# Performance work log

Hardware: AMD Instinct MI355X
Metric: run time of the kernel (lower is better)

## Reference

```python
import jax, jax.numpy as jnp
import numpy as np

N_SUBS = 64
INPUT_DIMS = 256
MIDDLE_DIMS = 128
OUTPUT_DIMS = 256
N = 131072


def setup_inputs() -> dict:
    key = jax.random.key(0)
    k1, k2 = jax.random.split(key)
    x = jax.random.normal(k1, (N, INPUT_DIMS), dtype=jnp.float32)
    sub = jax.random.randint(k2, (N,), 0, N_SUBS, dtype=jnp.int64 if jax.config.jax_enable_x64 else jnp.int32)
    # learned scalar params, initialized as in the torch module
    Gamma = jnp.ones((1,), jnp.float32) / (MIDDLE_DIMS * INPUT_DIMS)
    Lambda = jnp.ones((1,), jnp.float32) / (OUTPUT_DIMS * (INPUT_DIMS + MIDDLE_DIMS))
    return {"x": x, "sub": sub, "Gamma": Gamma, "Lambda": Lambda}


def reference(x, sub, Gamma, Lambda):
    # per-subject mean via fused segment reduction (replaces python loop)
    sums = jax.ops.segment_sum(x, sub, num_segments=N_SUBS)                      # [S, D_in]
    counts = jax.ops.segment_sum(jnp.ones((x.shape[0],), x.dtype), sub,
                                 num_segments=N_SUBS)[:, None]                    # [S, 1]
    # torch fallback for empty group: mean over row 0 of x
    means = jnp.where(counts > 0, sums / jnp.maximum(counts, 1), x[0][None, :])   # [S, D_in]
    # F.linear with rank-1 all-Gamma weight == Gamma * row-sum broadcast to middle dims
    s = jax.nn.relu(Gamma[0] * jnp.sum(means, axis=1, keepdims=True))             # [S, 1]
    stats = jnp.broadcast_to(s, (N_SUBS, MIDDLE_DIMS))                            # [S, D_mid]
    batch_stats = stats[sub]                                                      # [N, D_mid] gather
    cat = jnp.concatenate([x, batch_stats], axis=1)                               # [N, D_in+D_mid]
    o = jax.nn.relu(Lambda[0] * jnp.sum(cat, axis=1, keepdims=True))              # [N, 1]
    return jnp.broadcast_to(o, (x.shape[0], OUTPUT_DIMS))                         # [N, D_out]
```

## Files before the change

### kernel.cpp

```cpp
#include <hip/hip_runtime.h>

#define N_ROWS    131072
#define D_IN      256
#define D_MID     128
#define N_SUBS    64
#define K1_BLOCKS 4096
#define ROWS_PER_WAVE (N_ROWS / (K1_BLOCKS * 4))


__global__ __launch_bounds__(256) void k1_rowsum(const float* __restrict__ x,
                                                 float* __restrict__ rowsum,
                                                 float* __restrict__ bins) {
    if (blockIdx.x == 0 && threadIdx.x < 2 * N_SUBS) bins[threadIdx.x] = 0.0f;
    const int lane   = threadIdx.x & 63;
    const int waveId = blockIdx.x * 4 + (threadIdx.x >> 6);
    const int row0   = waveId * ROWS_PER_WAVE;
    const float4* __restrict__ xp = (const float4*)x;
    #pragma unroll
    for (int r = 0; r < ROWS_PER_WAVE; r += 4) {
        float4 a = xp[(size_t)(row0 + r + 0) * 64 + lane];
        float4 b = xp[(size_t)(row0 + r + 1) * 64 + lane];
        float4 c = xp[(size_t)(row0 + r + 2) * 64 + lane];
        float4 d = xp[(size_t)(row0 + r + 3) * 64 + lane];
        float s0 = (a.x + a.y) + (a.z + a.w);
        float s1 = (b.x + b.y) + (b.z + b.w);
        float s2 = (c.x + c.y) + (c.z + c.w);
        float s3 = (d.x + d.y) + (d.z + d.w);
        #pragma unroll
        for (int m = 32; m >= 1; m >>= 1) {
            s0 += __shfl_xor(s0, m, 64);
            s1 += __shfl_xor(s1, m, 64);
            s2 += __shfl_xor(s2, m, 64);
            s3 += __shfl_xor(s3, m, 64);
        }
        if (lane == 0)
            *(float4*)(rowsum + row0 + r) = make_float4(s0, s1, s2, s3);
    }
}

__global__ __launch_bounds__(256) void k2_group(const float* __restrict__ rowsum,
                                                const int* __restrict__ sub,
                                                float* __restrict__ gsum,
                                                float* __restrict__ gcnt) {
    __shared__ float ls[N_SUBS];
    __shared__ float lc[N_SUBS];
    if (threadIdx.x < N_SUBS) { ls[threadIdx.x] = 0.0f; lc[threadIdx.x] = 0.0f; }
    __syncthreads();
    int stride = gridDim.x * blockDim.x;
    for (int i = blockIdx.x * blockDim.x + threadIdx.x; i < N_ROWS; i += stride) {
        int g = sub[i];
        atomicAdd(&ls[g], rowsum[i]);
        atomicAdd(&lc[g], 1.0f);
    }
    __syncthreads();
    if (threadIdx.x < N_SUBS) {
        atomicAdd(&gsum[threadIdx.x], ls[threadIdx.x]);
        atomicAdd(&gcnt[threadIdx.x], lc[threadIdx.x]);
    }
}

__global__ __launch_bounds__(256) void k3_out(const float* __restrict__ rowsum,
                                              const int* __restrict__ sub,
                                              const float* __restrict__ gsum,
                                              const float* __restrict__ gcnt,
                                              const float* __restrict__ Gamma,
                                              const float* __restrict__ Lambda,
                                              float* __restrict__ out) {
    const int lane   = threadIdx.x & 63;
    const int waveId = blockIdx.x * 4 + (threadIdx.x >> 6);
    const int row0   = waveId * ROWS_PER_WAVE;
    const float G = Gamma[0], L = Lambda[0];
    const float rs0 = rowsum[0];
    #pragma unroll
    for (int r = 0; r < ROWS_PER_WAVE; ++r) {
        const int row = row0 + r;
        const int g   = sub[row];
        const float c  = gcnt[g];
        const float ms = (c > 0.0f) ? (gsum[g] / c) : rs0;
        const float s  = fmaxf(G * ms, 0.0f);
        const float o  = fmaxf(L * (rowsum[row] + (float)D_MID * s), 0.0f);
        ((float4*)(out + (size_t)row * D_IN))[lane] = make_float4(o, o, o, o);
    }
}

extern "C" void kernel_launch(void* const* d_in, const int* in_sizes, int n_in,
                              void* d_out, int out_size, void* d_ws, size_t ws_size,
                              hipStream_t stream) {
    const float* x      = (const float*)d_in[0];
    const int*   sub    = (const int*)d_in[1];
    const float* Gamma  = (const float*)d_in[2];
    const float* Lambda = (const float*)d_in[3];
    float* out = (float*)d_out;

    float* rowsum = (float*)d_ws;
    float* gsum   = rowsum + N_ROWS;
    float* gcnt   = gsum + N_SUBS;

    k1_rowsum<<<K1_BLOCKS, 256, 0, stream>>>(x, rowsum, gsum);
    k2_group<<<64, 256, 0, stream>>>(rowsum, sub, gsum, gcnt);
    k3_out<<<K1_BLOCKS, 256, 0, stream>>>(rowsum, sub, gsum, gcnt, Gamma, Lambda, out);
}
```

Baseline: 249.2 us.

## Fuse per-subject grouping into the row-sum kernel and shrink its grid

The separate group-reduction kernel is removed. Each wave now adds its row sums and counts into shared-memory bins right after reducing each row, and each block flushes its bins to global with atomics. The row-sum kernel launches 512 blocks with 64 rows per wave so those flush atomics stay few, and a memset replaces the in-kernel zeroing of the bins. This saves one launch and the re-read of rowsum, at the cost of fewer blocks in flight for the heavy streaming read of x and shared-memory atomic contention.

```diff
diff --git a/kernel.cpp b/kernel.cpp
--- a/kernel.cpp
+++ b/kernel.cpp
@@ -4,24 +4,36 @@
 #define D_IN      256
 #define D_MID     128
 #define N_SUBS    64
-#define K1_BLOCKS 4096
-#define ROWS_PER_WAVE (N_ROWS / (K1_BLOCKS * 4))
+
+#define K1_BLOCKS 512
+#define K1_ROWS_PER_WAVE (N_ROWS / (K1_BLOCKS * 4))
+#define K3_BLOCKS 4096
+#define K3_ROWS_PER_WAVE (N_ROWS / (K3_BLOCKS * 4))
 
 
-__global__ __launch_bounds__(256) void k1_rowsum(const float* __restrict__ x,
-                                                 float* __restrict__ rowsum,
-                                                 float* __restrict__ bins) {
-    if (blockIdx.x == 0 && threadIdx.x < 2 * N_SUBS) bins[threadIdx.x] = 0.0f;
+__global__ __launch_bounds__(256) void k1_rowsum_group(const float* __restrict__ x,
+                                                       const int* __restrict__ sub,
+                                                       float* __restrict__ rowsum,
+                                                       float* __restrict__ gsum,
+                                                       float* __restrict__ gcnt) {
+    __shared__ float lsum[N_SUBS];
+    __shared__ float lcnt[N_SUBS];
+    if (threadIdx.x < N_SUBS)            lsum[threadIdx.x] = 0.0f;
+    else if (threadIdx.x < 2 * N_SUBS)   lcnt[threadIdx.x - N_SUBS] = 0.0f;
+    __syncthreads();
+
     const int lane   = threadIdx.x & 63;
     const int waveId = blockIdx.x * 4 + (threadIdx.x >> 6);
-    const int row0   = waveId * ROWS_PER_WAVE;
+    const int row0   = waveId * K1_ROWS_PER_WAVE;
     const float4* __restrict__ xp = (const float4*)x;
-    #pragma unroll
-    for (int r = 0; r < ROWS_PER_WAVE; r += 4) {
-        float4 a = xp[(size_t)(row0 + r + 0) * 64 + lane];
-        float4 b = xp[(size_t)(row0 + r + 1) * 64 + lane];
-        float4 c = xp[(size_t)(row0 + r + 2) * 64 + lane];
-        float4 d = xp[(size_t)(row0 + r + 3) * 64 + lane];
+
+    #pragma unroll 4
+    for (int r = 0; r < K1_ROWS_PER_WAVE; r += 4) {
+        const int rb = row0 + r;
+        float4 a = xp[(size_t)(rb + 0) * 64 + lane];
+        float4 b = xp[(size_t)(rb + 1) * 64 + lane];
+        float4 c = xp[(size_t)(rb + 2) * 64 + lane];
+        float4 d = xp[(size_t)(rb + 3) * 64 + lane];
         float s0 = (a.x + a.y) + (a.z + a.w);
         float s1 = (b.x + b.y) + (b.z + b.w);
         float s2 = (c.x + c.y) + (c.z + c.w);
@@ -34,29 +46,19 @@
             s3 += __shfl_xor(s3, m, 64);
         }
         if (lane == 0)
-            *(float4*)(rowsum + row0 + r) = make_float4(s0, s1, s2, s3);
-    }
-}
-
-__global__ __launch_bounds__(256) void k2_group(const float* __restrict__ rowsum,
-                                                const int* __restrict__ sub,
-                                                float* __restrict__ gsum,
-                                                float* __restrict__ gcnt) {
-    __shared__ float ls[N_SUBS];
-    __shared__ float lc[N_SUBS];
-    if (threadIdx.x < N_SUBS) { ls[threadIdx.x] = 0.0f; lc[threadIdx.x] = 0.0f; }
-    __syncthreads();
-    int stride = gridDim.x * blockDim.x;
-    for (int i = blockIdx.x * blockDim.x + threadIdx.x; i < N_ROWS; i += stride) {
-        int g = sub[i];
-        atomicAdd(&ls[g], rowsum[i]);
-        atomicAdd(&lc[g], 1.0f);
+            *(float4*)(rowsum + rb) = make_float4(s0, s1, s2, s3);
+        if (lane < 4) {
+            float sv = (lane == 0) ? s0 : (lane == 1) ? s1 : (lane == 2) ? s2 : s3;
+            atomicAdd(&lsum[sub[rb + lane]], sv);
+        } else if (lane < 8) {
+            atomicAdd(&lcnt[sub[rb + (lane - 4)]], 1.0f);
+        }
     }
     __syncthreads();
-    if (threadIdx.x < N_SUBS) {
-        atomicAdd(&gsum[threadIdx.x], ls[threadIdx.x]);
-        atomicAdd(&gcnt[threadIdx.x], lc[threadIdx.x]);
-    }
+    if (threadIdx.x < N_SUBS)
+        atomicAdd(&gsum[threadIdx.x], lsum[threadIdx.x]);
+    else if (threadIdx.x < 2 * N_SUBS)
+        atomicAdd(&gcnt[threadIdx.x - N_SUBS], lcnt[threadIdx.x - N_SUBS]);
 }
 
 __global__ __launch_bounds__(256) void k3_out(const float* __restrict__ rowsum,
@@ -68,11 +70,11 @@
                                               float* __restrict__ out) {
     const int lane   = threadIdx.x & 63;
     const int waveId = blockIdx.x * 4 + (threadIdx.x >> 6);
-    const int row0   = waveId * ROWS_PER_WAVE;
+    const int row0   = waveId * K3_ROWS_PER_WAVE;
     const float G = Gamma[0], L = Lambda[0];
     const float rs0 = rowsum[0];
     #pragma unroll
-    for (int r = 0; r < ROWS_PER_WAVE; ++r) {
+    for (int r = 0; r < K3_ROWS_PER_WAVE; ++r) {
         const int row = row0 + r;
         const int g   = sub[row];
         const float c  = gcnt[g];
@@ -96,7 +98,7 @@
     float* gsum   = rowsum + N_ROWS;
     float* gcnt   = gsum + N_SUBS;
 
-    k1_rowsum<<<K1_BLOCKS, 256, 0, stream>>>(x, rowsum, gsum);
-    k2_group<<<64, 256, 0, stream>>>(rowsum, sub, gsum, gcnt);
-    k3_out<<<K1_BLOCKS, 256, 0, stream>>>(rowsum, sub, gsum, gcnt, Gamma, Lambda, out);
+    hipMemsetAsync(gsum, 0, 2 * N_SUBS * sizeof(float), stream);
+    k1_rowsum_group<<<K1_BLOCKS, 256, 0, stream>>>(x, sub, rowsum, gsum, gcnt);
+    k3_out<<<K3_BLOCKS, 256, 0, stream>>>(rowsum, sub, gsum, gcnt, Gamma, Lambda, out);
 }
```

Measured after the change: 253.0 us. No clear change (+1.5%).
